# Optimization experiments

Measured on AMD Instinct MI355X. Metric: run time of the kernel, lower is better.

Reference implementation:

```python
import jax, jax.numpy as jnp
import numpy as np

D_MODEL, D_MID, D_FEAT = 1024, 4096, 16384
K_MID, K_FEAT = 128, 64
K_AUX_MID, K_AUX_FEAT = 256, 512
BATCHES_TO_DEAD = 2
AUX_COEFF = 0.03125
B, S = 2, 1024


def _ku(key, fan_in, shape):
    # torch kaiming_uniform_ default (a=0): bound = sqrt(6/fan_in), fan_in = shape[1]
    bound = (6.0 / fan_in) ** 0.5
    return jax.random.uniform(key, shape, jnp.float32, -bound, bound)


def setup_inputs() -> dict:
    key = jax.random.key(0)
    ks = jax.random.split(key, 8)
    return {
        "x": jax.random.normal(ks[0], (B, S, D_MODEL), jnp.float32),
        "W_enc1": _ku(ks[1], D_MID, (D_MODEL, D_MID)),
        "b_enc1": jnp.zeros((D_MID,), jnp.float32),
        "W_enc2": _ku(ks[2], D_FEAT, (D_MID, D_FEAT)),
        "b_enc2": jnp.zeros((D_FEAT,), jnp.float32),
        "W_dec2": _ku(ks[3], D_MID, (D_FEAT, D_MID)),
        "b_dec2": jnp.zeros((D_MID,), jnp.float32),
        "W_dec1": _ku(ks[4], D_MODEL, (D_MID, D_MODEL)),
        "b_dec1": jnp.zeros((D_MODEL,), jnp.float32),
        "n_inactive_0": jax.random.randint(ks[5], (D_MID,), 0, 6, jnp.int32),
        "n_inactive_1": jax.random.randint(ks[6], (D_FEAT,), 0, 6, jnp.int32),
        "n_inactive_2": jax.random.randint(ks[7], (D_MID,), 0, 6, jnp.int32),
    }


def _scatter_last(vals, idx, out_shape):
    # scatter vals at idx along last axis into zeros of out_shape
    n = int(np.prod(out_shape[:-1]))
    k = idx.shape[-1]
    out = jnp.zeros((n, out_shape[-1]), vals.dtype)
    out = out.at[jnp.arange(n)[:, None], idx.reshape(n, k)].set(vals.reshape(n, k))
    return out.reshape(out_shape)


def _topk_mask(x, k):
    vals, idx = jax.lax.top_k(x, k)
    return _scatter_last(vals, idx, x.shape)


def reference(x, W_enc1, b_enc1, W_enc2, b_enc2, W_dec2, b_dec2, W_dec1, b_dec1,
              n_inactive_0, n_inactive_1, n_inactive_2):
    x = x.astype(jnp.float32)
    inp = jax.lax.stop_gradient(x)  # input = x.clone().detach()
    pre0 = jax.nn.relu(x @ W_enc1 + b_enc1)          # [B,S,d_mid]
    mid0 = _topk_mask(pre0, K_MID)
    pre1 = jax.nn.relu(mid0 @ W_enc2 + b_enc2)       # [B,S,d_feat]
    mid1 = _topk_mask(pre1, K_FEAT)
    pre2 = jax.nn.relu(mid1 @ W_dec2 + b_dec2)       # [B,S,d_mid]
    mid2 = _topk_mask(pre2, K_MID)
    recon = mid2 @ W_dec1 + b_dec1                   # [B,S,d_model]

    # _update_n_inactive (happens before the loss uses the buffers)
    def upd(c, act):
        s = jnp.sum(act, axis=(0, 1))
        return jnp.where(s > 0, 0.0, c.astype(jnp.float32) + (s == 0).astype(jnp.float32))
    counters = [upd(n_inactive_0, mid0), upd(n_inactive_1, mid1), upd(n_inactive_2, mid2)]

    l2_loss = jnp.mean((recon - inp) ** 2)
    residual = inp - recon
    layers = [(W_enc2, b_enc2, K_FEAT), (W_dec2, b_dec2, K_MID), (W_dec1, b_dec1, None)]
    aux_loss = jnp.float32(0.0)
    for i, (cnt, acts, k_aux) in enumerate(zip(counters, [pre0, pre1, pre2],
                                               [K_AUX_MID, K_AUX_FEAT, K_AUX_MID])):
        dead = cnt > BATCHES_TO_DEAD  # [d]
        # top-k restricted to dead features: mask live features to -inf, then
        # scatter + relu zeroes any -inf picks. Zeros at live features make the
        # full-width matmul equal to the original W[dead_feats] gathered matmul.
        masked = jnp.where(dead, acts, -jnp.inf)
        vals, idx = jax.lax.top_k(masked, k_aux)
        h = jax.nn.relu(_scatter_last(vals, idx, acts.shape))
        for (W, b, kk) in layers[i:]:
            h = h @ W + b
            if kk is not None:
                h = _topk_mask(jax.nn.relu(h), kk)
        term = jnp.mean((h - residual) ** 2)
        aux_loss = aux_loss + jnp.where(jnp.any(dead), term, 0.0)

    loss = l2_loss + AUX_COEFF * aux_loss
    return recon, loss, l2_loss, aux_loss
```

## Files before the change

### kernel.cpp

```cpp
#include <hip/hip_runtime.h>
#include <cstddef>
#include <cstdint>

#define N_ROWS 2048
#define DM 1024
#define DMID 4096
#define DFEAT 16384

using u32 = unsigned int;

__device__ __forceinline__ float relu_pos(float v) { return v > 0.f ? v : 0.f; }

__global__ void init_zero_kernel(int* a0, int* a1, int* a2, float* fs, int* is) {
  int t = blockIdx.x * 256 + threadIdx.x;
  if (t < DFEAT) a1[t] = 0;
  if (t < DMID) { a0[t] = 0; a2[t] = 0; }
  if (t < 4) { fs[t] = 0.f; is[t] = 0; }
}

__global__ __launch_bounds__(256) void gemm_relu_kernel(
    const float* __restrict__ A, const float* __restrict__ W,
    const float* __restrict__ bias, float* __restrict__ C,
    int M, int N, int K)
{
  __shared__ float As[16][132];
  __shared__ float Bs[16][132];
  const int tid = threadIdx.x;
  const int bn0 = blockIdx.x * 128;
  const int bm0 = blockIdx.y * 128;
  const int tx = tid & 15, ty = tid >> 4;
  float acc[8][8];
#pragma unroll
  for (int m = 0; m < 8; ++m)
#pragma unroll
    for (int n = 0; n < 8; ++n) acc[m][n] = 0.f;

  for (int k0 = 0; k0 < K; k0 += 16) {
#pragma unroll
    for (int it = 0; it < 2; ++it) {
      int li = tid + it * 256;
      int rr = li >> 2;
      int cc = (li & 3) << 2;
      float4 a = *(const float4*)&A[(size_t)(bm0 + rr) * K + k0 + cc];
      As[cc + 0][rr] = a.x; As[cc + 1][rr] = a.y;
      As[cc + 2][rr] = a.z; As[cc + 3][rr] = a.w;
    }
#pragma unroll
    for (int it = 0; it < 2; ++it) {
      int li = tid + it * 256;
      int rr = li >> 5;
      int cc = (li & 31) << 2;
      *(float4*)&Bs[rr][cc] = *(const float4*)&W[(size_t)(k0 + rr) * N + bn0 + cc];
    }
    __syncthreads();
#pragma unroll
    for (int kk = 0; kk < 16; ++kk) {
      float av[8], bv[8];
      *(float4*)&av[0] = *(const float4*)&As[kk][ty * 8];
      *(float4*)&av[4] = *(const float4*)&As[kk][ty * 8 + 4];
      *(float4*)&bv[0] = *(const float4*)&Bs[kk][tx * 8];
      *(float4*)&bv[4] = *(const float4*)&Bs[kk][tx * 8 + 4];
#pragma unroll
      for (int m = 0; m < 8; ++m)
#pragma unroll
        for (int n = 0; n < 8; ++n) acc[m][n] += av[m] * bv[n];
    }
    __syncthreads();
  }
#pragma unroll
  for (int m = 0; m < 8; ++m) {
    int rrow = bm0 + ty * 8 + m;
#pragma unroll
    for (int n4 = 0; n4 < 8; n4 += 4) {
      int ccol = bn0 + tx * 8 + n4;
      float4 o;
      o.x = relu_pos(acc[m][n4 + 0] + bias[ccol + 0]);
      o.y = relu_pos(acc[m][n4 + 1] + bias[ccol + 1]);
      o.z = relu_pos(acc[m][n4 + 2] + bias[ccol + 2]);
      o.w = relu_pos(acc[m][n4 + 3] + bias[ccol + 3]);
      *(float4*)&C[(size_t)rrow * N + ccol] = o;
    }
  }
}

template<int NW, bool DEAD>
__global__ __launch_bounds__(NW * 64) void topk_kernel(
    const float* __restrict__ src, int k, const int* __restrict__ dead,
    int* __restrict__ oidx, float* __restrict__ oval, int* __restrict__ ocnt)
{
  constexpr int B = NW * 64;
  constexpr int E = 16;
  const int tid = threadIdx.x;
  const int r = blockIdx.x;
  __shared__ int red[NW + 1];
  __shared__ int cnt_s, eq_s;
  u32 keys[E];
  const float* row = src + (size_t)r * (B * E);
#pragma unroll
  for (int j = 0; j < E; ++j) {
    int i = tid + j * B;
    float v = row[i];
    if (DEAD) keys[j] = dead[i] ? (__float_as_uint(v) + 1u) : 0u;
    else      keys[j] = __float_as_uint(v);
  }
  auto count_gt = [&](u32 x) -> int {
    int c = 0;
#pragma unroll
    for (int j = 0; j < E; ++j) c += (keys[j] > x) ? 1 : 0;
#pragma unroll
    for (int o = 32; o > 0; o >>= 1) c += __shfl_down(c, o, 64);
    if ((tid & 63) == 0) red[tid >> 6] = c;
    __syncthreads();
    if (tid == 0) {
      int t = 0;
#pragma unroll
      for (int w = 0; w < NW; ++w) t += red[w];
      red[NW] = t;
    }
    __syncthreads();
    return red[NW];
  };
  const u32 baseKey = DEAD ? 1u : 0u;
  int ck = count_gt(baseKey);
  u32 T;
  int take = 0;
  if (ck >= k) {
    u32 M = 0;
    for (int b = 30; b >= 0; --b) {
      u32 cand = M | (1u << b);
      int c = count_gt(cand);
      if (c >= k) M = cand;
    }
    T = M + 1u;
    int G = count_gt(T);
    take = (T > baseKey) ? (k - G) : 0;
  } else {
    T = baseKey;
  }
  if (tid == 0) { cnt_s = 0; eq_s = 0; }
  __syncthreads();
#pragma unroll
  for (int j = 0; j < E; ++j) {
    u32 kk = keys[j];
    if (kk > T) {
      int s = atomicAdd(&cnt_s, 1);
      oidx[(size_t)r * k + s] = tid + j * B;
      oval[(size_t)r * k + s] = __uint_as_float(DEAD ? (kk - 1u) : kk);
    }
  }
  __syncthreads();
  if (take > 0) {
#pragma unroll
    for (int j = 0; j < E; ++j) {
      if (keys[j] == T) {
        int e = atomicAdd(&eq_s, 1);
        if (e < take) {
          int s = atomicAdd(&cnt_s, 1);
          oidx[(size_t)r * k + s] = tid + j * B;
          oval[(size_t)r * k + s] = __uint_as_float(DEAD ? (T - 1u) : T);
        }
      }
    }
    __syncthreads();
  }
  if (tid == 0) ocnt[r] = cnt_s;
}

__global__ __launch_bounds__(256) void spmm_kernel(
    const int* __restrict__ sidx, const float* __restrict__ sval,
    const int* __restrict__ scnt, int kslots,
    const float* __restrict__ W, int ncols,
    const float* __restrict__ bias, float* __restrict__ out, int do_relu)
{
  __shared__ int si[512];
  __shared__ float sv[512];
  const int r = blockIdx.x;
  const int n = scnt[r];
  for (int i = threadIdx.x; i < n; i += 256) {
    si[i] = sidx[(size_t)r * kslots + i];
    sv[i] = sval[(size_t)r * kslots + i];
  }
  __syncthreads();
  const int c0 = blockIdx.y * 1024 + threadIdx.x * 4;
  float4 acc = *(const float4*)&bias[c0];
  for (int j = 0; j < n; ++j) {
    float v = sv[j];
    const float4 w = *(const float4*)&W[(size_t)si[j] * ncols + c0];
    acc.x += v * w.x; acc.y += v * w.y; acc.z += v * w.z; acc.w += v * w.w;
  }
  if (do_relu) {
    acc.x = relu_pos(acc.x); acc.y = relu_pos(acc.y);
    acc.z = relu_pos(acc.z); acc.w = relu_pos(acc.w);
  }
  *(float4*)&out[(size_t)r * ncols + c0] = acc;
}

__global__ __launch_bounds__(256) void spmm_term_kernel(
    const int* __restrict__ sidx, const float* __restrict__ sval,
    const int* __restrict__ scnt, int kslots,
    const float* __restrict__ W, const float* __restrict__ bias,
    const float* __restrict__ x, const float* __restrict__ recon,
    float* __restrict__ accum)
{
  __shared__ int si[512];
  __shared__ float sv[512];
  __shared__ float redf[4];
  const int r = blockIdx.x;
  const int n = scnt[r];
  for (int i = threadIdx.x; i < n; i += 256) {
    si[i] = sidx[(size_t)r * kslots + i];
    sv[i] = sval[(size_t)r * kslots + i];
  }
  __syncthreads();
  const int c0 = threadIdx.x * 4;
  float4 acc = *(const float4*)&bias[c0];
  for (int j = 0; j < n; ++j) {
    float v = sv[j];
    const float4 w = *(const float4*)&W[(size_t)si[j] * 1024 + c0];
    acc.x += v * w.x; acc.y += v * w.y; acc.z += v * w.z; acc.w += v * w.w;
  }
  const float4 xx = *(const float4*)&x[(size_t)r * 1024 + c0];
  const float4 rc = *(const float4*)&recon[(size_t)r * 1024 + c0];
  float d0 = acc.x - (xx.x - rc.x);
  float d1 = acc.y - (xx.y - rc.y);
  float d2 = acc.z - (xx.z - rc.z);
  float d3 = acc.w - (xx.w - rc.w);
  float local = d0 * d0 + d1 * d1 + d2 * d2 + d3 * d3;
#pragma unroll
  for (int o = 32; o > 0; o >>= 1) local += __shfl_down(local, o, 64);
  if ((threadIdx.x & 63) == 0) redf[threadIdx.x >> 6] = local;
  __syncthreads();
  if (threadIdx.x == 0) atomicAdd(accum, redf[0] + redf[1] + redf[2] + redf[3]);
}

__global__ __launch_bounds__(256) void l2_kernel(
    const float* __restrict__ x, const float* __restrict__ recon,
    float* __restrict__ accum)
{
  __shared__ float redf[4];
  const int r = blockIdx.x;
  const int c0 = threadIdx.x * 4;
  const float4 xx = *(const float4*)&x[(size_t)r * 1024 + c0];
  const float4 rc = *(const float4*)&recon[(size_t)r * 1024 + c0];
  float d0 = rc.x - xx.x, d1 = rc.y - xx.y, d2 = rc.z - xx.z, d3 = rc.w - xx.w;
  float local = d0 * d0 + d1 * d1 + d2 * d2 + d3 * d3;
#pragma unroll
  for (int o = 32; o > 0; o >>= 1) local += __shfl_down(local, o, 64);
  if ((threadIdx.x & 63) == 0) redf[threadIdx.x >> 6] = local;
  __syncthreads();
  if (threadIdx.x == 0) atomicAdd(accum, redf[0] + redf[1] + redf[2] + redf[3]);
}

__global__ void mark_active_kernel(const int* __restrict__ idx, const int* __restrict__ cnt,
                                   int kslots, int* __restrict__ active)
{
  const int r = blockIdx.x;
  const int s = threadIdx.x;
  if (s < cnt[r]) active[idx[(size_t)r * kslots + s]] = 1;
}

__global__ void dead_kernel(const int* __restrict__ active, const int* __restrict__ ni,
                            int* __restrict__ dead, int* __restrict__ anyflag)
{
  const int j = blockIdx.x * 256 + threadIdx.x;
  int isdead = (active[j] == 0 && ni[j] >= 2) ? 1 : 0;
  dead[j] = isdead;
  if (isdead) atomicOr(anyflag, 1);
}

__global__ void finalize_kernel(const float* __restrict__ fs, const int* __restrict__ is,
                                float* __restrict__ out)
{
  if (blockIdx.x == 0 && threadIdx.x == 0) {
    const float inv = 1.0f / 2097152.0f;
    float l2 = fs[0] * inv;
    float aux = 0.f;
    if (is[0]) aux += fs[1] * inv;
    if (is[1]) aux += fs[2] * inv;
    if (is[2]) aux += fs[3] * inv;
    out[2097152] = l2 + 0.03125f * aux;
    out[2097153] = l2;
    out[2097154] = aux;
  }
}

extern "C" void kernel_launch(void* const* d_in, const int* in_sizes, int n_in,
                              void* d_out, int out_size, void* d_ws, size_t ws_size,
                              hipStream_t stream)
{
  (void)in_sizes; (void)n_in; (void)out_size; (void)ws_size;
  const float* x      = (const float*)d_in[0];
  const float* W_enc1 = (const float*)d_in[1];
  const float* b_enc1 = (const float*)d_in[2];
  const float* W_enc2 = (const float*)d_in[3];
  const float* b_enc2 = (const float*)d_in[4];
  const float* W_dec2 = (const float*)d_in[5];
  const float* b_dec2 = (const float*)d_in[6];
  const float* W_dec1 = (const float*)d_in[7];
  const float* b_dec1 = (const float*)d_in[8];
  const int* ni0 = (const int*)d_in[9];
  const int* ni1 = (const int*)d_in[10];
  const int* ni2 = (const int*)d_in[11];
  float* out = (float*)d_out;

  char* ws = (char*)d_ws;
  size_t cur = 0;
  auto carve = [&](size_t bytes) -> void* {
    void* p = ws + cur;
    cur += (bytes + 255) & ~(size_t)255;
    return p;
  };
  float* pre0 = (float*)carve((size_t)N_ROWS * DMID * 4);
  float* pre2 = (float*)carve((size_t)N_ROWS * DMID * 4);
  float* pre1 = (float*)carve((size_t)N_ROWS * DFEAT * 4);

  int*   idx0 = (int*)carve((size_t)N_ROWS * 128 * 4);
  float* val0 = (float*)carve((size_t)N_ROWS * 128 * 4);
  int*   cnt0 = (int*)carve((size_t)N_ROWS * 4);
  int*   idx1 = (int*)carve((size_t)N_ROWS * 64 * 4);
  float* val1 = (float*)carve((size_t)N_ROWS * 64 * 4);
  int*   cnt1 = (int*)carve((size_t)N_ROWS * 4);
  int*   idx2 = (int*)carve((size_t)N_ROWS * 128 * 4);
  float* val2 = (float*)carve((size_t)N_ROWS * 128 * 4);
  int*   cnt2 = (int*)carve((size_t)N_ROWS * 4);

  int*   h0i = (int*)carve((size_t)N_ROWS * 256 * 4);
  float* h0v = (float*)carve((size_t)N_ROWS * 256 * 4);
  int*   h0c = (int*)carve((size_t)N_ROWS * 4);
  int*   h1i = (int*)carve((size_t)N_ROWS * 512 * 4);
  float* h1v = (float*)carve((size_t)N_ROWS * 512 * 4);
  int*   h1c = (int*)carve((size_t)N_ROWS * 4);
  int*   h2i = (int*)carve((size_t)N_ROWS * 256 * 4);
  float* h2v = (float*)carve((size_t)N_ROWS * 256 * 4);
  int*   h2c = (int*)carve((size_t)N_ROWS * 4);

  int*   t0i  = (int*)carve((size_t)N_ROWS * 64 * 4);
  float* t0v  = (float*)carve((size_t)N_ROWS * 64 * 4);
  int*   t0c  = (int*)carve((size_t)N_ROWS * 4);
  int*   t0bi = (int*)carve((size_t)N_ROWS * 128 * 4);
  float* t0bv = (float*)carve((size_t)N_ROWS * 128 * 4);
  int*   t0bc = (int*)carve((size_t)N_ROWS * 4);
  int*   t1bi = (int*)carve((size_t)N_ROWS * 128 * 4);
  float* t1bv = (float*)carve((size_t)N_ROWS * 128 * 4);
  int*   t1bc = (int*)carve((size_t)N_ROWS * 4);

  int* active0 = (int*)carve(DMID * 4);
  int* active1 = (int*)carve(DFEAT * 4);
  int* active2 = (int*)carve(DMID * 4);
  int* dead0   = (int*)carve(DMID * 4);
  int* dead1   = (int*)carve(DFEAT * 4);
  int* dead2   = (int*)carve(DMID * 4);
  float* fscal = (float*)carve(64);
  int*   iscal = (int*)carve(64);

  init_zero_kernel<<<64, 256, 0, stream>>>(active0, active1, active2, fscal, iscal);

  gemm_relu_kernel<<<dim3(DMID / 128, N_ROWS / 128), 256, 0, stream>>>(
      x, W_enc1, b_enc1, pre0, N_ROWS, DMID, DM);
  topk_kernel<4, false><<<N_ROWS, 256, 0, stream>>>(pre0, 128, nullptr, idx0, val0, cnt0);
  spmm_kernel<<<dim3(N_ROWS, DFEAT / 1024), 256, 0, stream>>>(
      idx0, val0, cnt0, 128, W_enc2, DFEAT, b_enc2, pre1, 1);
  topk_kernel<16, false><<<N_ROWS, 1024, 0, stream>>>(pre1, 64, nullptr, idx1, val1, cnt1);
  spmm_kernel<<<dim3(N_ROWS, DMID / 1024), 256, 0, stream>>>(
      idx1, val1, cnt1, 64, W_dec2, DMID, b_dec2, pre2, 1);
  topk_kernel<4, false><<<N_ROWS, 256, 0, stream>>>(pre2, 128, nullptr, idx2, val2, cnt2);
  spmm_kernel<<<dim3(N_ROWS, 1), 256, 0, stream>>>(
      idx2, val2, cnt2, 128, W_dec1, DM, b_dec1, out, 0);

  l2_kernel<<<N_ROWS, 256, 0, stream>>>(x, out, &fscal[0]);

  mark_active_kernel<<<N_ROWS, 128, 0, stream>>>(idx0, cnt0, 128, active0);
  mark_active_kernel<<<N_ROWS, 64, 0, stream>>>(idx1, cnt1, 64, active1);
  mark_active_kernel<<<N_ROWS, 128, 0, stream>>>(idx2, cnt2, 128, active2);
  dead_kernel<<<DMID / 256, 256, 0, stream>>>(active0, ni0, dead0, &iscal[0]);
  dead_kernel<<<DFEAT / 256, 256, 0, stream>>>(active1, ni1, dead1, &iscal[1]);
  dead_kernel<<<DMID / 256, 256, 0, stream>>>(active2, ni2, dead2, &iscal[2]);

  topk_kernel<4, true><<<N_ROWS, 256, 0, stream>>>(pre0, 256, dead0, h0i, h0v, h0c);
  topk_kernel<16, true><<<N_ROWS, 1024, 0, stream>>>(pre1, 512, dead1, h1i, h1v, h1c);
  topk_kernel<4, true><<<N_ROWS, 256, 0, stream>>>(pre2, 256, dead2, h2i, h2v, h2c);

  spmm_kernel<<<dim3(N_ROWS, DFEAT / 1024), 256, 0, stream>>>(
      h0i, h0v, h0c, 256, W_enc2, DFEAT, b_enc2, pre1 , 1);
  topk_kernel<16, false><<<N_ROWS, 1024, 0, stream>>>(pre1, 64, nullptr, t0i, t0v, t0c);
  spmm_kernel<<<dim3(N_ROWS, DMID / 1024), 256, 0, stream>>>(
      t0i, t0v, t0c, 64, W_dec2, DMID, b_dec2, pre0 , 1);
  topk_kernel<4, false><<<N_ROWS, 256, 0, stream>>>(pre0, 128, nullptr, t0bi, t0bv, t0bc);
  spmm_term_kernel<<<N_ROWS, 256, 0, stream>>>(
      t0bi, t0bv, t0bc, 128, W_dec1, b_dec1, x, out, &fscal[1]);

  spmm_kernel<<<dim3(N_ROWS, DMID / 1024), 256, 0, stream>>>(
      h1i, h1v, h1c, 512, W_dec2, DMID, b_dec2, pre0 , 1);
  topk_kernel<4, false><<<N_ROWS, 256, 0, stream>>>(pre0, 128, nullptr, t1bi, t1bv, t1bc);
  spmm_term_kernel<<<N_ROWS, 256, 0, stream>>>(
      t1bi, t1bv, t1bc, 128, W_dec1, b_dec1, x, out, &fscal[2]);

  spmm_term_kernel<<<N_ROWS, 256, 0, stream>>>(
      h2i, h2v, h2c, 256, W_dec1, b_dec1, x, out, &fscal[3]);

  finalize_kernel<<<1, 64, 0, stream>>>(fscal, iscal, out);
}
```

Before: 3.068 ms.

## Add XCD-aware column-sliced SpMM kernel with 4-way unrolled gathers

Adds a new sparse-times-dense kernel in which each block handles 4 rows and one 256-column slice. Block IDs are mapped so each XCD owns a contiguous set of column slices, which keeps the gathered weight columns resident in that XCD's L2. Output is written with nontemporal stores, and the gather loops in all SpMM kernels are unrolled by 4 so more loads are in flight. The risk is smaller per-block work, and shared-memory staging of up to 512 slots across 4 rows.

```diff
diff --git a/kernel.cpp b/kernel.cpp
--- a/kernel.cpp
+++ b/kernel.cpp
@@ -8,6 +8,7 @@
 #define DFEAT 16384
 
 using u32 = unsigned int;
+typedef float f32x4 __attribute__((ext_vector_type(4)));
 
 __device__ __forceinline__ float relu_pos(float v) { return v > 0.f ? v : 0.f; }
 
@@ -183,9 +184,23 @@
   __syncthreads();
   const int c0 = blockIdx.y * 1024 + threadIdx.x * 4;
   float4 acc = *(const float4*)&bias[c0];
-  for (int j = 0; j < n; ++j) {
+  const float* Wb = W + c0;
+  int j = 0;
+  for (; j + 4 <= n; j += 4) {
+    int   i0 = si[j],     i1 = si[j + 1], i2 = si[j + 2], i3 = si[j + 3];
+    float v0 = sv[j],     v1 = sv[j + 1], v2 = sv[j + 2], v3 = sv[j + 3];
+    const float4 w0 = *(const float4*)&Wb[(size_t)i0 * ncols];
+    const float4 w1 = *(const float4*)&Wb[(size_t)i1 * ncols];
+    const float4 w2 = *(const float4*)&Wb[(size_t)i2 * ncols];
+    const float4 w3 = *(const float4*)&Wb[(size_t)i3 * ncols];
+    acc.x += v0 * w0.x; acc.y += v0 * w0.y; acc.z += v0 * w0.z; acc.w += v0 * w0.w;
+    acc.x += v1 * w1.x; acc.y += v1 * w1.y; acc.z += v1 * w1.z; acc.w += v1 * w1.w;
+    acc.x += v2 * w2.x; acc.y += v2 * w2.y; acc.z += v2 * w2.z; acc.w += v2 * w2.w;
+    acc.x += v3 * w3.x; acc.y += v3 * w3.y; acc.z += v3 * w3.z; acc.w += v3 * w3.w;
+  }
+  for (; j < n; ++j) {
     float v = sv[j];
-    const float4 w = *(const float4*)&W[(size_t)si[j] * ncols + c0];
+    const float4 w = *(const float4*)&Wb[(size_t)si[j] * ncols];
     acc.x += v * w.x; acc.y += v * w.y; acc.z += v * w.z; acc.w += v * w.w;
   }
   if (do_relu) {
@@ -193,6 +208,69 @@
     acc.z = relu_pos(acc.z); acc.w = relu_pos(acc.w);
   }
   *(float4*)&out[(size_t)r * ncols + c0] = acc;
+}
+
+template<int KSLOTS>
+__global__ __launch_bounds__(256) void spmm4_kernel(
+    const int* __restrict__ sidx, const float* __restrict__ sval,
+    const int* __restrict__ scnt,
+    const float* __restrict__ W, int ncols,
+    const float* __restrict__ bias, float* __restrict__ out, int do_relu,
+    int nslices, int nrowblk)
+{
+  __shared__ int   si[4][KSLOTS];
+  __shared__ float sv[4][KSLOTS];
+  __shared__ int   cnts[4];
+
+  const int b   = blockIdx.x;
+  const int xcd = b & 7;
+  const int n   = b >> 3;
+  const int spx = nslices >> 3;
+  const int slice  = xcd * spx + (n / nrowblk);
+  const int rowblk = n % nrowblk;
+
+  const int tid = threadIdx.x;
+  const int r0 = rowblk * 4;
+  if (tid < 4) cnts[tid] = scnt[r0 + tid];
+  for (int i = tid; i < 4 * KSLOTS; i += 256) {
+    int rl = i / KSLOTS, sl = i % KSLOTS;
+    si[rl][sl] = sidx[(size_t)(r0 + rl) * KSLOTS + sl];
+    sv[rl][sl] = sval[(size_t)(r0 + rl) * KSLOTS + sl];
+  }
+  __syncthreads();
+
+  const int w = tid >> 6, lane = tid & 63;
+  const int row = r0 + w;
+  const int c = slice * 256 + lane * 4;
+  float4 acc = *(const float4*)&bias[c];
+  const int nn = cnts[w];
+  const float* Wb = W + c;
+
+  int j = 0;
+  for (; j + 4 <= nn; j += 4) {
+    int   i0 = si[w][j],     i1 = si[w][j + 1], i2 = si[w][j + 2], i3 = si[w][j + 3];
+    float v0 = sv[w][j],     v1 = sv[w][j + 1], v2 = sv[w][j + 2], v3 = sv[w][j + 3];
+    const float4 w0 = *(const float4*)&Wb[(size_t)i0 * ncols];
+    const float4 w1 = *(const float4*)&Wb[(size_t)i1 * ncols];
+    const float4 w2 = *(const float4*)&Wb[(size_t)i2 * ncols];
+    const float4 w3 = *(const float4*)&Wb[(size_t)i3 * ncols];
+    acc.x += v0 * w0.x; acc.y += v0 * w0.y; acc.z += v0 * w0.z; acc.w += v0 * w0.w;
+    acc.x += v1 * w1.x; acc.y += v1 * w1.y; acc.z += v1 * w1.z; acc.w += v1 * w1.w;
+    acc.x += v2 * w2.x; acc.y += v2 * w2.y; acc.z += v2 * w2.z; acc.w += v2 * w2.w;
+    acc.x += v3 * w3.x; acc.y += v3 * w3.y; acc.z += v3 * w3.z; acc.w += v3 * w3.w;
+  }
+  for (; j < nn; ++j) {
+    float v = sv[w][j];
+    const float4 ww = *(const float4*)&Wb[(size_t)si[w][j] * ncols];
+    acc.x += v * ww.x; acc.y += v * ww.y; acc.z += v * ww.z; acc.w += v * ww.w;
+  }
+  if (do_relu) {
+    acc.x = relu_pos(acc.x); acc.y = relu_pos(acc.y);
+    acc.z = relu_pos(acc.z); acc.w = relu_pos(acc.w);
+  }
+  f32x4 o;
+  o.x = acc.x; o.y = acc.y; o.z = acc.z; o.w = acc.w;
+  __builtin_nontemporal_store(o, (f32x4*)&out[(size_t)row * ncols + c]);
 }
 
 __global__ __launch_bounds__(256) void spmm_term_kernel(
@@ -214,9 +292,23 @@
   __syncthreads();
   const int c0 = threadIdx.x * 4;
   float4 acc = *(const float4*)&bias[c0];
-  for (int j = 0; j < n; ++j) {
+  const float* Wb = W + c0;
+  int j = 0;
+  for (; j + 4 <= n; j += 4) {
+    int   i0 = si[j],     i1 = si[j + 1], i2 = si[j + 2], i3 = si[j + 3];
+    float v0 = sv[j],     v1 = sv[j + 1], v2 = sv[j + 2], v3 = sv[j + 3];
+    const float4 w0 = *(const float4*)&Wb[(size_t)i0 * 1024];
+    const float4 w1 = *(const float4*)&Wb[(size_t)i1 * 1024];
+    const float4 w2 = *(const float4*)&Wb[(size_t)i2 * 1024];
+    const float4 w3 = *(const float4*)&Wb[(size_t)i3 * 1024];
+    acc.x += v0 * w0.x; acc.y += v0 * w0.y; acc.z += v0 * w0.z; acc.w += v0 * w0.w;
+    acc.x += v1 * w1.x; acc.y += v1 * w1.y; acc.z += v1 * w1.z; acc.w += v1 * w1.w;
+    acc.x += v2 * w2.x; acc.y += v2 * w2.y; acc.z += v2 * w2.z; acc.w += v2 * w2.w;
+    acc.x += v3 * w3.x; acc.y += v3 * w3.y; acc.z += v3 * w3.z; acc.w += v3 * w3.w;
+  }
+  for (; j < n; ++j) {
     float v = sv[j];
-    const float4 w = *(const float4*)&W[(size_t)si[j] * 1024 + c0];
+    const float4 w = *(const float4*)&Wb[(size_t)si[j] * 1024];
     acc.x += v * w.x; acc.y += v * w.y; acc.z += v * w.z; acc.w += v * w.w;
   }
   const float4 xx = *(const float4*)&x[(size_t)r * 1024 + c0];
@@ -358,11 +450,11 @@
   gemm_relu_kernel<<<dim3(DMID / 128, N_ROWS / 128), 256, 0, stream>>>(
       x, W_enc1, b_enc1, pre0, N_ROWS, DMID, DM);
   topk_kernel<4, false><<<N_ROWS, 256, 0, stream>>>(pre0, 128, nullptr, idx0, val0, cnt0);
-  spmm_kernel<<<dim3(N_ROWS, DFEAT / 1024), 256, 0, stream>>>(
-      idx0, val0, cnt0, 128, W_enc2, DFEAT, b_enc2, pre1, 1);
+  spmm4_kernel<128><<<(DFEAT / 256) * (N_ROWS / 4), 256, 0, stream>>>(
+      idx0, val0, cnt0, W_enc2, DFEAT, b_enc2, pre1, 1, DFEAT / 256, N_ROWS / 4);
   topk_kernel<16, false><<<N_ROWS, 1024, 0, stream>>>(pre1, 64, nullptr, idx1, val1, cnt1);
-  spmm_kernel<<<dim3(N_ROWS, DMID / 1024), 256, 0, stream>>>(
-      idx1, val1, cnt1, 64, W_dec2, DMID, b_dec2, pre2, 1);
+  spmm4_kernel<64><<<(DMID / 256) * (N_ROWS / 4), 256, 0, stream>>>(
+      idx1, val1, cnt1, W_dec2, DMID, b_dec2, pre2, 1, DMID / 256, N_ROWS / 4);
   topk_kernel<4, false><<<N_ROWS, 256, 0, stream>>>(pre2, 128, nullptr, idx2, val2, cnt2);
   spmm_kernel<<<dim3(N_ROWS, 1), 256, 0, stream>>>(
       idx2, val2, cnt2, 128, W_dec1, DM, b_dec1, out, 0);
@@ -380,17 +472,17 @@
   topk_kernel<16, true><<<N_ROWS, 1024, 0, stream>>>(pre1, 512, dead1, h1i, h1v, h1c);
   topk_kernel<4, true><<<N_ROWS, 256, 0, stream>>>(pre2, 256, dead2, h2i, h2v, h2c);
 
-  spmm_kernel<<<dim3(N_ROWS, DFEAT / 1024), 256, 0, stream>>>(
-      h0i, h0v, h0c, 256, W_enc2, DFEAT, b_enc2, pre1 , 1);
+  spmm4_kernel<256><<<(DFEAT / 256) * (N_ROWS / 4), 256, 0, stream>>>(
+      h0i, h0v, h0c, W_enc2, DFEAT, b_enc2, pre1 , 1, DFEAT / 256, N_ROWS / 4);
   topk_kernel<16, false><<<N_ROWS, 1024, 0, stream>>>(pre1, 64, nullptr, t0i, t0v, t0c);
-  spmm_kernel<<<dim3(N_ROWS, DMID / 1024), 256, 0, stream>>>(
-      t0i, t0v, t0c, 64, W_dec2, DMID, b_dec2, pre0 , 1);
+  spmm4_kernel<64><<<(DMID / 256) * (N_ROWS / 4), 256, 0, stream>>>(
+      t0i, t0v, t0c, W_dec2, DMID, b_dec2, pre0 , 1, DMID / 256, N_ROWS / 4);
   topk_kernel<4, false><<<N_ROWS, 256, 0, stream>>>(pre0, 128, nullptr, t0bi, t0bv, t0bc);
   spmm_term_kernel<<<N_ROWS, 256, 0, stream>>>(
       t0bi, t0bv, t0bc, 128, W_dec1, b_dec1, x, out, &fscal[1]);
 
-  spmm_kernel<<<dim3(N_ROWS, DMID / 1024), 256, 0, stream>>>(
-      h1i, h1v, h1c, 512, W_dec2, DMID, b_dec2, pre0 , 1);
+  spmm4_kernel<512><<<(DMID / 256) * (N_ROWS / 4), 256, 0, stream>>>(
+      h1i, h1v, h1c, W_dec2, DMID, b_dec2, pre0 , 1, DMID / 256, N_ROWS / 4);
   topk_kernel<4, false><<<N_ROWS, 256, 0, stream>>>(pre0, 128, nullptr, t1bi, t1bv, t1bc);
   spmm_term_kernel<<<N_ROWS, 256, 0, stream>>>(
       t1bi, t1bv, t1bc, 128, W_dec1, b_dec1, x, out, &fscal[2]);
```

Result: faster. 2.526 ms (-17.7%).
